# Kernel tuning notes

Measured on AMD Instinct MI355X. Metric: run time of the kernel, lower is better.

Reference implementation:

```python
import jax, jax.numpy as jnp
import numpy as np

B, C, D, T = 64, 512, 32, 32
DT = D * T
K = 128            # valid_num: top-K proposals kept for NMS-style pooling
MARGIN = 0.2       # opt.global_margin
MAX_VIOLATION = True
EPS = 1e-8         # torch.cosine_similarity eps


def _l2n(x, axis):
    # torch cosine_similarity normalizes each vector by max(||x||, eps)
    return x / jnp.maximum(jnp.linalg.norm(x, axis=axis, keepdims=True), EPS)


def _cos(a, b, axis):
    return jnp.sum(_l2n(a, axis) * _l2n(b, axis), axis=axis)


def setup_inputs() -> dict:
    key = jax.random.key(0)
    k1, k2, k3 = jax.random.split(key, 3)
    videos = jax.random.normal(k1, (B, C, D, T), jnp.float32)
    sentences = jax.random.normal(k2, (B, C), jnp.float32)
    iou = jax.random.uniform(k3, (DT, DT), jnp.float32)
    iou_maps = 0.5 * (iou + iou.T)
    iou_maps = iou_maps.at[jnp.arange(DT), jnp.arange(DT)].set(1.0)
    mask = jnp.ones((D, T), jnp.float32)
    lam = jnp.asarray(0.125, jnp.float32)
    return {"videos": videos, "sentences": sentences, "lam": lam,
            "mask": mask, "valid_num": K, "iou_maps": iou_maps}


def reference(videos, sentences, lam, mask, valid_num, iou_maps):
    b, c, d, t = videos.shape
    dt = d * t
    # center over channel dim (dim=1 in torch)
    V = videos - jnp.mean(videos, axis=1, keepdims=True)          # [b,c,d,t]
    S = sentences - jnp.mean(sentences, axis=1, keepdims=True)    # [b,c]
    Vf = V.reshape(b, c, dt)
    Vn = _l2n(Vf, axis=1)                                         # unit over c
    Sn = _l2n(S, axis=1)
    mflat = mask.reshape(dt)

    # cosine sim of every sentence vs every video proposal: [b_sent, b_vid, dt]
    cross = jnp.einsum('ic,jcp->ijp', Sn, Vn)
    cross = jnp.where(mflat == 0, -jnp.inf, cross)

    # --- per-sample positive pooling (loop 1) ---
    self_score = cross[jnp.arange(b), jnp.arange(b)]              # [b, dt]
    w = jax.nn.softmax(self_score, axis=-1)
    video_pos = jnp.einsum('bp,bcp->bc', w, Vf)                   # [b, c]

    # sentence-sentence sims + hard negative mining
    sim = Sn @ Sn.T                                               # [b, b]
    idx = jnp.argsort(-sim, axis=1)                               # descending
    neg_idx = idx[:, 6:b - 5]                                     # b > 11 path
    neg_sents = S[neg_idx]                                        # [b, b-11, c]
    pos_score = _cos(video_pos, S, axis=1)                        # [b]
    neg_score = _cos(video_pos[:, None, :], neg_sents, axis=2)    # [b, b-11]
    vas_loss = jnp.mean(jax.nn.relu(MARGIN + neg_score - pos_score[:, None]), axis=1).mean()

    # cross-video pseudo-positive (crov), gated on nearest-neighbor sim > 0.9
    nn_idx = idx[:, 1]
    pse = Vf[nn_idx]                                              # [b, c, dt]
    vsim = jax.nn.softmax(_cos(video_pos[:, :, None], pse, axis=1), axis=-1)  # [b, dt]
    p_v = jnp.einsum('bp,bcp->bc', vsim, pse)
    n_v = jnp.einsum('bp,bcp->bc', (1.0 - vsim) * mflat, pse) / (valid_num - 1)
    crov = jax.nn.relu(MARGIN + _cos(video_pos, n_v, axis=1) - _cos(video_pos, p_v, axis=1))
    gate = sim[jnp.arange(b), nn_idx] > 0.9
    crov_loss = jnp.where(gate, crov, 0.0).mean()

    # --- NMS-weighted video score pooling (loop 2) ---
    pmap = self_score.reshape(b, d, t)                            # postive_map
    topv, topi = jax.lax.top_k(cross, valid_num)                  # [b,b,K]
    # pairwise IoU among the top-K proposals of each (sentence, video) pair
    iou = iou_maps[topi[..., :, None], topi[..., None, :]]        # [b,b,K,K]
    lower = jnp.tril(jnp.ones((valid_num, valid_num), bool), -1)  # l < k
    decay = jnp.prod(1.0 - jnp.where(lower, iou, 0.0), axis=-1)   # [b,b,K]
    wk = jax.nn.softmax(lam * topv, axis=-1)
    scores = jnp.sum(wk * decay * topv, axis=-1)                  # [b,b]

    # bidirectional margin ranking loss
    diag = jnp.diag(scores)[:, None]
    eye = jnp.eye(b, dtype=bool)
    cost_s = jnp.where(eye, 0.0, jax.nn.relu(MARGIN + scores - diag))
    cost_im = jnp.where(eye, 0.0, jax.nn.relu(MARGIN + scores - diag.T))
    if MAX_VIOLATION:
        cost_s = cost_s.max(axis=1)
        cost_im = cost_im.max(axis=0)
    loss = cost_s.sum() / b + cost_im.sum() / b + vas_loss + crov_loss
    return loss, pmap
```

## Files before the change

kernel.cpp:

```cpp
#include <hip/hip_runtime.h>
#include <hip/hip_fp16.h>
#include <math.h>

#define BB 64
#define CC 512
#define DTT 1024
#define NNEG 53
#define MARGIN_ 0.2f
#define EPSV 1e-8f
#define LDB 132

typedef short s16x8 __attribute__((ext_vector_type(8)));
typedef float f32x4 __attribute__((ext_vector_type(4)));

__device__ __forceinline__ float bred_sum(float v, float* red, int tid, int nt) {
  red[tid] = v; __syncthreads();
  for (int s = nt >> 1; s > 0; s >>= 1) { if (tid < s) red[tid] += red[tid + s]; __syncthreads(); }
  float r = red[0]; __syncthreads();
  return r;
}
__device__ __forceinline__ float bred_max(float v, float* red, int tid, int nt) {
  red[tid] = v; __syncthreads();
  for (int s = nt >> 1; s > 0; s >>= 1) { if (tid < s) red[tid] = fmaxf(red[tid], red[tid + s]); __syncthreads(); }
  float r = red[0]; __syncthreads();
  return r;
}

__global__ void k_sent(const float* __restrict__ sent, float* __restrict__ Sn,
                       unsigned short* __restrict__ SnH, unsigned short* __restrict__ SnL,
                       float* __restrict__ SnSum) {
  int b = blockIdx.x, tid = threadIdx.x;
  __shared__ float red[256];
  float x0 = sent[b * CC + tid], x1 = sent[b * CC + tid + 256];
  float mean = bred_sum(x0 + x1, red, tid, 256) * (1.0f / CC);
  float s0 = x0 - mean, s1 = x1 - mean;
  float ss = bred_sum(s0 * s0 + s1 * s1, red, tid, 256);
  float nrm = fmaxf(sqrtf(ss), EPSV);
  float n0 = s0 / nrm, n1 = s1 / nrm;
  Sn[b * CC + tid] = n0; Sn[b * CC + tid + 256] = n1;
  unsigned u0 = __float_as_uint(n0), u1 = __float_as_uint(n1);
  SnH[b * CC + tid] = (unsigned short)(u0 >> 16);
  SnH[b * CC + tid + 256] = (unsigned short)(u1 >> 16);
  float l0 = n0 - __uint_as_float(u0 & 0xFFFF0000u);
  float l1 = n1 - __uint_as_float(u1 & 0xFFFF0000u);
  SnL[b * CC + tid] = (unsigned short)(__float_as_uint(l0) >> 16);
  SnL[b * CC + tid + 256] = (unsigned short)(__float_as_uint(l1) >> 16);
  float sn = bred_sum(n0 + n1, red, tid, 256);
  if (tid == 0) SnSum[b] = sn;
}

__global__ void k_sim(const float* __restrict__ Sn, int* __restrict__ nn_idx,
                      int* __restrict__ negidx, float* __restrict__ nnsim) {
  int i = blockIdx.x, j = threadIdx.x;
  float dot = 0.f;
  for (int c = 0; c < CC; ++c) dot += Sn[i * CC + c] * Sn[j * CC + c];
  __shared__ float srow[BB];
  srow[j] = dot; __syncthreads();
  float mv = srow[j];
  int rank = 0;
  for (int k = 0; k < BB; ++k) {
    float vk = srow[k];
    if (vk > mv || (vk == mv && k < j)) rank++;
  }
  if (rank == 1) { nn_idx[i] = j; nnsim[i] = mv; }
  if (rank >= 6 && rank < 59) negidx[i * NNEG + rank - 6] = j;
}

__global__ void k_prep_iou(const float* __restrict__ iou, __half* __restrict__ L16) {
  int g = (blockIdx.x * 256 + threadIdx.x) * 4;
  float4 x = *(const float4*)(iou + g);
  __half2 h0 = __floats2half2_rn(1.f - x.x, 1.f - x.y);
  __half2 h1 = __floats2half2_rn(1.f - x.z, 1.f - x.w);
  *(__half2*)(L16 + g) = h0;
  *(__half2*)(L16 + g + 2) = h1;
}

__global__ __launch_bounds__(256) void k_cross(const float* __restrict__ videos,
    const unsigned short* __restrict__ SnH, const unsigned short* __restrict__ SnL,
    const float* __restrict__ SnSum, const float* __restrict__ mask,
    float* __restrict__ cross, float* __restrict__ meanv, float* __restrict__ normv) {
  __shared__ unsigned int BH[2][16][LDB];
  __shared__ unsigned int BL[2][16][LDB];
  __shared__ float SnSum_s[64];
  __shared__ float mb_s[128];
  __shared__ float inv_s[128];

  int tid = threadIdx.x;
  int j = blockIdx.x >> 3;
  int p0 = (blockIdx.x & 7) << 7;
  int lane = tid & 63;
  int wv = tid >> 6;
  int row = lane & 15;
  int g = lane >> 4;
  int g8 = g << 3;
  int pA = wv << 5;

  int kp = tid >> 4;
  int pb = (tid & 15) << 3;

  const float* vbase = videos + ((size_t)j * CC) * DTT + p0;

  f32x4 acc[4][2];
#pragma unroll
  for (int a = 0; a < 4; ++a)
#pragma unroll
    for (int pf = 0; pf < 2; ++pf)
#pragma unroll
      for (int r = 0; r < 4; ++r) acc[a][pf][r] = 0.f;

  float sacc[8], ssacc[8];
#pragma unroll
  for (int q = 0; q < 8; ++q) { sacc[q] = 0.f; ssacc[q] = 0.f; }

  const float* pr = vbase + (size_t)(2 * kp) * DTT + pb;
  float4 f0 = *(const float4*)(pr);
  float4 f1 = *(const float4*)(pr + 4);
  float4 f2 = *(const float4*)(pr + DTT);
  float4 f3 = *(const float4*)(pr + DTT + 4);

#pragma unroll
  for (int t = 0; t < 16; ++t) {
    int kc = t * 32;
    int cb = t & 1;
    s16x8 AH[4], AL[4];
#pragma unroll
    for (int a = 0; a < 4; ++a) {
      int off = (a * 16 + row) * CC + kc + g8;
      AH[a] = *(const s16x8*)(SnH + off);
      AL[a] = *(const s16x8*)(SnL + off);
    }
    {
      float xe[8] = {f0.x, f0.y, f0.z, f0.w, f1.x, f1.y, f1.z, f1.w};
      float xo[8] = {f2.x, f2.y, f2.z, f2.w, f3.x, f3.y, f3.z, f3.w};
      unsigned int hw[8], lw[8];
#pragma unroll
      for (int q = 0; q < 8; ++q) {
        unsigned ue = __float_as_uint(xe[q]);
        unsigned uo = __float_as_uint(xo[q]);
        hw[q] = (ue >> 16) | (uo & 0xFFFF0000u);
        float el = xe[q] - __uint_as_float(ue & 0xFFFF0000u);
        float ol = xo[q] - __uint_as_float(uo & 0xFFFF0000u);
        lw[q] = (__float_as_uint(el) >> 16) | (__float_as_uint(ol) & 0xFFFF0000u);
        sacc[q] += xe[q] + xo[q];
        ssacc[q] = fmaf(xe[q], xe[q], ssacc[q]);
        ssacc[q] = fmaf(xo[q], xo[q], ssacc[q]);
      }
      *(uint4*)&BH[cb][kp][pb]     = make_uint4(hw[0], hw[1], hw[2], hw[3]);
      *(uint4*)&BH[cb][kp][pb + 4] = make_uint4(hw[4], hw[5], hw[6], hw[7]);
      *(uint4*)&BL[cb][kp][pb]     = make_uint4(lw[0], lw[1], lw[2], lw[3]);
      *(uint4*)&BL[cb][kp][pb + 4] = make_uint4(lw[4], lw[5], lw[6], lw[7]);
    }
    if (t + 1 < 16) {
      const float* pn = vbase + (size_t)((t + 1) * 32 + 2 * kp) * DTT + pb;
      f0 = *(const float4*)(pn);
      f1 = *(const float4*)(pn + 4);
      f2 = *(const float4*)(pn + DTT);
      f3 = *(const float4*)(pn + DTT + 4);
    }
    __syncthreads();
#pragma unroll
    for (int pf = 0; pf < 2; ++pf) {
      int p = pA + pf * 16 + row;
      int kpb = g << 2;
      union { unsigned int u[4]; s16x8 v; } bh, bl;
      bh.u[0] = BH[cb][kpb][p]; bh.u[1] = BH[cb][kpb + 1][p];
      bh.u[2] = BH[cb][kpb + 2][p]; bh.u[3] = BH[cb][kpb + 3][p];
      bl.u[0] = BL[cb][kpb][p]; bl.u[1] = BL[cb][kpb + 1][p];
      bl.u[2] = BL[cb][kpb + 2][p]; bl.u[3] = BL[cb][kpb + 3][p];
#pragma unroll
      for (int a = 0; a < 4; ++a) {
        acc[a][pf] = __builtin_amdgcn_mfma_f32_16x16x32_bf16(AH[a], bh.v, acc[a][pf], 0, 0, 0);
        acc[a][pf] = __builtin_amdgcn_mfma_f32_16x16x32_bf16(AH[a], bl.v, acc[a][pf], 0, 0, 0);
        acc[a][pf] = __builtin_amdgcn_mfma_f32_16x16x32_bf16(AL[a], bh.v, acc[a][pf], 0, 0, 0);
      }
    }
  }

  float (*Sred)[LDB] = (float(*)[LDB])&BH[0][0][0];
  float (*SSred)[LDB] = (float(*)[LDB])&BL[0][0][0];
#pragma unroll
  for (int q = 0; q < 8; ++q) { Sred[kp][pb + q] = sacc[q]; SSred[kp][pb + q] = ssacc[q]; }
  if (tid < 64) SnSum_s[tid] = SnSum[tid];
  __syncthreads();
  if (tid < 128) {
    float s = 0.f, ss = 0.f;
#pragma unroll
    for (int k = 0; k < 16; ++k) { s += Sred[k][tid]; ss += SSred[k][tid]; }
    float mb = s * (1.0f / CC);
    float var = ss - s * mb;
    float nrm = fmaxf(sqrtf(fmaxf(var, 0.f)), EPSV);
    meanv[j * DTT + p0 + tid] = mb;
    normv[j * DTT + p0 + tid] = nrm;
    mb_s[tid] = mb;
    inv_s[tid] = 1.f / nrm;
  }
  __syncthreads();

#pragma unroll
  for (int pf = 0; pf < 2; ++pf) {
    int p = pA + pf * 16 + row;
    float mb = mb_s[p], inv = inv_s[p];
    float mk = mask[p0 + p];
#pragma unroll
    for (int a = 0; a < 4; ++a) {
#pragma unroll
      for (int r = 0; r < 4; ++r) {
        int i = a * 16 + (g << 2) + r;
        float val = (acc[a][pf][r] - mb * SnSum_s[i]) * inv;
        if (mk == 0.f) val = -INFINITY;
        cross[((size_t)i * BB + j) * DTT + p0 + p] = val;
      }
    }
  }
}

__global__ void k_softmax_w(const float* __restrict__ cross, const float* __restrict__ meanv,
                            float* __restrict__ pmap, float* __restrict__ w, float* __restrict__ wm) {
  int b = blockIdx.x, tid = threadIdx.x;
  __shared__ float red[256];
  const float* row = cross + ((size_t)b * BB + b) * DTT;
  float v[4]; float mx = -INFINITY;
#pragma unroll
  for (int q = 0; q < 4; ++q) {
    v[q] = row[q * 256 + tid];
    pmap[b * DTT + q * 256 + tid] = v[q];
    mx = fmaxf(mx, v[q]);
  }
  mx = bred_max(mx, red, tid, 256);
  float e[4]; float se = 0.f;
#pragma unroll
  for (int q = 0; q < 4; ++q) { e[q] = expf(v[q] - mx); se += e[q]; }
  se = bred_sum(se, red, tid, 256);
  float inv = 1.f / se;
  float wmacc = 0.f;
#pragma unroll
  for (int q = 0; q < 4; ++q) {
    float wv = e[q] * inv;
    w[b * DTT + q * 256 + tid] = wv;
    wmacc += wv * meanv[b * DTT + q * 256 + tid];
  }
  wmacc = bred_sum(wmacc, red, tid, 256);
  if (tid == 0) wm[b] = wmacc;
}

__global__ void k_vpos(const float* __restrict__ videos, const float* __restrict__ w,
                       const float* __restrict__ wm, float* __restrict__ vp) {
  int wid = (blockIdx.x * 256 + threadIdx.x) >> 6;
  int lane = threadIdx.x & 63;
  int b = wid >> 9, c = wid & 511;
  const float4* vb = (const float4*)(videos + (size_t)(b * CC + c) * DTT) + lane * 4;
  const float4* wb = (const float4*)(w + b * DTT) + lane * 4;
  float acc = 0.f;
#pragma unroll
  for (int q = 0; q < 4; ++q) {
    float4 x = vb[q], y = wb[q];
    acc += x.x * y.x + x.y * y.y + x.z * y.z + x.w * y.w;
  }
#pragma unroll
  for (int off = 32; off > 0; off >>= 1) acc += __shfl_xor(acc, off);
  if (lane == 0) vp[b * CC + c] = acc - wm[b];
}

__global__ void k_vpnorm(const float* __restrict__ vp, float* __restrict__ vpn,
                         float* __restrict__ vpsum) {
  int b = blockIdx.x, tid = threadIdx.x;
  __shared__ float red[256];
  float x0 = vp[b * CC + tid], x1 = vp[b * CC + tid + 256];
  float ss = bred_sum(x0 * x0 + x1 * x1, red, tid, 256);
  float sm = bred_sum(x0 + x1, red, tid, 256);
  if (tid == 0) { vpn[b] = fmaxf(sqrtf(ss), EPSV); vpsum[b] = sm; }
}

__global__ void k_vsim_logits(const float* __restrict__ videos, const float* __restrict__ vp,
    const float* __restrict__ vpn, const float* __restrict__ vpsum, const int* __restrict__ nn_idx,
    const float* __restrict__ meanv, const float* __restrict__ normv, float* __restrict__ vslog) {
  int gid = blockIdx.x * 256 + threadIdx.x;
  int b = gid >> 10, p = gid & 1023;
  int nn = nn_idx[b];
  const float* base = videos + (size_t)nn * CC * DTT + p;
  const float* vpr = vp + b * CC;
  float acc = 0.f;
#pragma unroll 1
  for (int c0 = 0; c0 < CC; c0 += 16) {
    float v[16];
#pragma unroll
    for (int u = 0; u < 16; ++u) v[u] = base[(size_t)(c0 + u) * DTT];
#pragma unroll
    for (int u = 0; u < 16; ++u) acc = fmaf(vpr[c0 + u], v[u], acc);
  }
  acc -= meanv[nn * DTT + p] * vpsum[b];
  vslog[gid] = acc / (vpn[b] * normv[nn * DTT + p]);
}

__global__ void k_softmax_vsim(float* __restrict__ vslog, const int* __restrict__ nn_idx,
    const float* __restrict__ meanv, const float* __restrict__ mask,
    float* __restrict__ svp, float* __restrict__ svn) {
  int b = blockIdx.x, tid = threadIdx.x;
  __shared__ float red[256];
  int nn = nn_idx[b];
  float v[4]; float mx = -INFINITY;
#pragma unroll
  for (int q = 0; q < 4; ++q) { v[q] = vslog[b * DTT + q * 256 + tid]; mx = fmaxf(mx, v[q]); }
  mx = bred_max(mx, red, tid, 256);
  float e[4]; float se = 0.f;
#pragma unroll
  for (int q = 0; q < 4; ++q) { e[q] = expf(v[q] - mx); se += e[q]; }
  se = bred_sum(se, red, tid, 256);
  float inv = 1.f / se;
  float sp = 0.f, sn2 = 0.f;
#pragma unroll
  for (int q = 0; q < 4; ++q) {
    int p = q * 256 + tid;
    float vs = e[q] * inv;
    vslog[b * DTT + p] = vs;
    float mm = meanv[nn * DTT + p];
    sp += vs * mm;
    sn2 += (1.f - vs) * mask[p] * mm;
  }
  sp = bred_sum(sp, red, tid, 256);
  sn2 = bred_sum(sn2, red, tid, 256);
  if (tid == 0) { svp[b] = sp; svn[b] = sn2; }
}

__global__ void k_pvnv(const float* __restrict__ videos, const float* __restrict__ vsim,
    const int* __restrict__ nn_idx, const float* __restrict__ mask,
    const float* __restrict__ svp, const float* __restrict__ svn, const int* __restrict__ vn_p,
    float* __restrict__ pv, float* __restrict__ nv) {
  int wid = (blockIdx.x * 256 + threadIdx.x) >> 6;
  int lane = threadIdx.x & 63;
  int b = wid >> 9, c = wid & 511;
  int nn = nn_idx[b];
  const float4* vb = (const float4*)(videos + (size_t)(nn * CC + c) * DTT) + lane * 4;
  const float4* vs4 = (const float4*)(vsim + b * DTT) + lane * 4;
  const float4* m4 = ((const float4*)mask) + lane * 4;
  float ap = 0.f, an = 0.f;
#pragma unroll
  for (int q = 0; q < 4; ++q) {
    float4 x = vb[q], s = vs4[q], m = m4[q];
    ap += x.x * s.x + x.y * s.y + x.z * s.z + x.w * s.w;
    an += x.x * (1.f - s.x) * m.x + x.y * (1.f - s.y) * m.y + x.z * (1.f - s.z) * m.z + x.w * (1.f - s.w) * m.w;
  }
#pragma unroll
  for (int off = 32; off > 0; off >>= 1) { ap += __shfl_xor(ap, off); an += __shfl_xor(an, off); }
  if (lane == 0) {
    float kd = (float)(*vn_p - 1);
    pv[b * CC + c] = ap - svp[b];
    nv[b * CC + c] = (an - svn[b]) / kd;
  }
}

__global__ void k_vas(const float* __restrict__ vp, const float* __restrict__ vpn,
                      const float* __restrict__ Sn, const int* __restrict__ negidx,
                      float* __restrict__ vasrow) {
  int i = blockIdx.x, tid = threadIdx.x;
  __shared__ float red[64];
  __shared__ float pos;
  float invn = 1.f / vpn[i];
  float val = 0.f;
  if (tid < NNEG) {
    int nj = negidx[i * NNEG + tid];
    float d = 0.f;
    for (int c = 0; c < CC; ++c) d += vp[i * CC + c] * Sn[nj * CC + c];
    val = d * invn;
  }
  if (tid == 63) {
    float d = 0.f;
    for (int c = 0; c < CC; ++c) d += vp[i * CC + c] * Sn[i * CC + c];
    pos = d * invn;
  }
  __syncthreads();
  float contrib = (tid < NNEG) ? fmaxf(MARGIN_ + val - pos, 0.f) : 0.f;
  float s = bred_sum(contrib, red, tid, 64);
  if (tid == 0) vasrow[i] = s / (float)NNEG;
}

__global__ void k_crov(const float* __restrict__ vp, const float* __restrict__ vpn,
                       const float* __restrict__ pv, const float* __restrict__ nv,
                       const float* __restrict__ nnsim, float* __restrict__ crovrow) {
  int b = blockIdx.x, tid = threadIdx.x;
  __shared__ float red[256];
  float dp = 0.f, pp = 0.f, dn = 0.f, nn2 = 0.f;
  for (int c = tid; c < CC; c += 256) {
    float a = vp[b * CC + c], x = pv[b * CC + c], y = nv[b * CC + c];
    dp += a * x; pp += x * x; dn += a * y; nn2 += y * y;
  }
  dp = bred_sum(dp, red, tid, 256);
  pp = bred_sum(pp, red, tid, 256);
  dn = bred_sum(dn, red, tid, 256);
  nn2 = bred_sum(nn2, red, tid, 256);
  if (tid == 0) {
    float cosp = dp / (vpn[b] * fmaxf(sqrtf(pp), EPSV));
    float cosn = dn / (vpn[b] * fmaxf(sqrtf(nn2), EPSV));
    float crov = fmaxf(MARGIN_ + cosn - cosp, 0.f);
    crovrow[b] = (nnsim[b] > 0.9f) ? crov : 0.f;
  }
}

__global__ __launch_bounds__(256) void k_select(const float* __restrict__ cross,
    const int* __restrict__ vn_p, unsigned* __restrict__ ordi_g, float* __restrict__ ordv_g) {
  __shared__ unsigned int hist_s[4][256];
  __shared__ unsigned int sel_s[4][128];
  __shared__ unsigned int selk_s[4][128];
  __shared__ unsigned int cnt_s[4];
  int tid = threadIdx.x;
  int wv = tid >> 6, lane = tid & 63;
  int ij = blockIdx.x * 4 + wv;
  int K = *vn_p; if (K > 128) K = 128;
  unsigned int* hist = hist_s[wv];
  unsigned int* sel = sel_s[wv];
  unsigned int* selk = selk_s[wv];

  const float* row = cross + (size_t)ij * DTT;
  unsigned int v[16];
#pragma unroll
  for (int q = 0; q < 16; ++q) {
    unsigned u = __float_as_uint(row[q * 64 + lane]);
    v[q] = (u & 0x80000000u) ? ~u : (u | 0x80000000u);
  }
  if (lane == 0) cnt_s[wv] = 0u;
  __builtin_amdgcn_wave_barrier();

  unsigned prefix = 0u, pmask = 0u;
  int remaining = K;
  for (int shift = 24; shift >= 0; shift -= 8) {
#pragma unroll
    for (int q = 0; q < 4; ++q) hist[lane * 4 + q] = 0u;
    __builtin_amdgcn_wave_barrier();
#pragma unroll
    for (int q = 0; q < 16; ++q) {
      if ((v[q] & pmask) == prefix)
        atomicAdd(&hist[(v[q] >> shift) & 255u], 1u);
    }
    __builtin_amdgcn_wave_barrier();
    unsigned c0 = hist[lane * 4], c1 = hist[lane * 4 + 1];
    unsigned c2 = hist[lane * 4 + 2], c3 = hist[lane * 4 + 3];
    unsigned s = c0 + c1 + c2 + c3;
    unsigned inc = s;
#pragma unroll
    for (int off = 1; off < 64; off <<= 1) {
      unsigned t = __shfl_down(inc, off);
      if (lane + off < 64) inc += t;
    }
    unsigned exc = inc - s;
    bool found = (exc < (unsigned)remaining) && (inc >= (unsigned)remaining);
    unsigned long long bmask = __ballot(found);
    int winner = (int)(__ffsll((unsigned long long)bmask) - 1);
    unsigned packed = 0u;
    if (found) {
      unsigned c = exc;
      unsigned cc[4] = {c0, c1, c2, c3};
      int d = lane * 4;
#pragma unroll
      for (int q = 3; q >= 0; --q) {
        if (c + cc[q] >= (unsigned)remaining) { d = lane * 4 + q; break; }
        c += cc[q];
      }
      packed = ((unsigned)d << 16) | (unsigned)(remaining - (int)c);
    }
    packed = __shfl(packed, winner);
    prefix |= (packed >> 16) << shift;
    remaining = (int)(packed & 0xFFFFu);
    pmask |= 255u << shift;
  }

#pragma unroll
  for (int q = 0; q < 16; ++q) {
    if (v[q] > prefix) {
      unsigned pos = atomicAdd(&cnt_s[wv], 1u);
      sel[pos] = (unsigned)(q * 64 + lane);
      selk[pos] = v[q];
    }
  }
  __builtin_amdgcn_wave_barrier();
  {
    int base = K - remaining;
    int last = -1;
    for (int t = 0; t < remaining; ++t) {
      int mymin = 0x7FFFFFFF;
#pragma unroll
      for (int q = 0; q < 16; ++q) {
        int idx = q * 64 + lane;
        if (v[q] == prefix && idx > last && idx < mymin) mymin = idx;
      }
#pragma unroll
      for (int off = 32; off > 0; off >>= 1) mymin = min(mymin, __shfl_xor(mymin, off));
      if (lane == 0) { sel[base + t] = (unsigned)mymin; selk[base + t] = prefix; }
      last = mymin;
    }
  }
  __builtin_amdgcn_wave_barrier();

  for (int e = lane; e < K; e += 64) {
    unsigned myidx = sel[e], myk = selk[e];
    int rank = 0;
    for (int m = 0; m < K; ++m) {
      unsigned ok = selk[m];
      rank += (ok > myk || (ok == myk && sel[m] < myidx)) ? 1 : 0;
    }
    unsigned u = (myk & 0x80000000u) ? (myk & 0x7FFFFFFFu) : ~myk;
    ordi_g[ij * 128 + rank] = myidx;
    ordv_g[ij * 128 + rank] = __uint_as_float(u);
  }
}

__global__ __launch_bounds__(256) void k_decay(const __half* __restrict__ L16,
    const unsigned* __restrict__ ordi_g, const float* __restrict__ ordv_g,
    const float* __restrict__ lam_p, const int* __restrict__ vn_p,
    float* __restrict__ scores) {
  __shared__ unsigned ti[128];
  __shared__ float dks[128];
  int ij = blockIdx.x, tid = threadIdx.x;
  int wv = tid >> 6, lane = tid & 63;
  int K = *vn_p; if (K > 128) K = 128;
  float lam = *lam_p;
  if (tid < 128) {
    ti[tid] = (tid < K) ? ordi_g[ij * 128 + tid] : 0u;
    dks[tid] = 1.f;
  }
  __syncthreads();

  for (int r = wv; r < K; r += 4) {
    const __half* irow = L16 + (size_t)ti[r] * DTT;
    float f = 1.f;
    if (lane < r && lane < 64) f = __half2float(irow[ti[lane]]);
    float prod = f;
#pragma unroll
    for (int off = 32; off > 0; off >>= 1) prod *= __shfl_xor(prod, off);
    if (r > 64 && prod > 1e-14f) {
      float f2 = 1.f;
      int m = 64 + lane;
      if (m < r) f2 = __half2float(irow[ti[m]]);
#pragma unroll
      for (int off = 32; off > 0; off >>= 1) f2 *= __shfl_xor(f2, off);
      prod *= f2;
    }
    if (lane == 0) dks[r] = prod;
  }
  __syncthreads();

  if (wv == 0) {
    bool okA = (lane < K), okB = (lane + 64 < K);
    float vA = okA ? ordv_g[ij * 128 + lane] : 0.f;
    float vB = okB ? ordv_g[ij * 128 + lane + 64] : 0.f;
    float mx = fmaxf(okA ? lam * vA : -INFINITY, okB ? lam * vB : -INFINITY);
#pragma unroll
    for (int off = 32; off > 0; off >>= 1) mx = fmaxf(mx, __shfl_xor(mx, off));
    float eA = okA ? expf(lam * vA - mx) : 0.f;
    float eB = okB ? expf(lam * vB - mx) : 0.f;
    float se = eA + eB;
    float sc = (okA ? eA * dks[lane] * vA : 0.f) + (okB ? eB * dks[lane + 64] * vB : 0.f);
#pragma unroll
    for (int off = 32; off > 0; off >>= 1) {
      se += __shfl_xor(se, off);
      sc += __shfl_xor(sc, off);
    }
    if (lane == 0) scores[ij] = sc / se;
  }
}

__global__ void k_final(const float* __restrict__ scores, const float* __restrict__ vasrow,
                        const float* __restrict__ crovrow, float* __restrict__ out) {
  int tid = threadIdx.x;
  __shared__ float sm[BB * BB];
  __shared__ float red[64];
  for (int q = tid; q < BB * BB; q += 64) sm[q] = scores[q];
  __syncthreads();
  float di = sm[tid * BB + tid];
  float rowmax = 0.f, colmax = 0.f;
  for (int k = 0; k < BB; ++k) {
    if (k != tid) {
      rowmax = fmaxf(rowmax, fmaxf(MARGIN_ + sm[tid * BB + k] - di, 0.f));
      colmax = fmaxf(colmax, fmaxf(MARGIN_ + sm[k * BB + tid] - di, 0.f));
    }
  }
  float total = bred_sum(rowmax + colmax + vasrow[tid] + crovrow[tid], red, tid, 64);
  if (tid == 0) out[0] = total * (1.0f / BB);
}

extern "C" void kernel_launch(void* const* d_in, const int* in_sizes, int n_in,
                              void* d_out, int out_size, void* d_ws, size_t ws_size,
                              hipStream_t stream) {
  const float* videos = (const float*)d_in[0];
  const float* sentences = (const float*)d_in[1];
  const float* lam = (const float*)d_in[2];
  const float* mask = (const float*)d_in[3];
  const int* valid_num = (const int*)d_in[4];
  const float* iou_maps = (const float*)d_in[5];
  float* out = (float*)d_out;
  float* pmap = out + 1;

  float* ws = (float*)d_ws;
  float* Sn = ws;
  float* SnT_unused = Sn + 32768;
  float* SnSum = SnT_unused + 32768;
  float* meanv = SnSum + 64;
  float* normv = meanv + 65536;
  float* cross = normv + 65536;
  float* w = cross + 4194304;
  float* wm = w + 65536;
  float* vp = wm + 64;
  float* vpn = vp + 32768;
  float* vpsum = vpn + 64;
  float* nnsim = vpsum + 64;
  float* vslog = nnsim + 64;
  float* svp = vslog + 65536;
  float* svn = svp + 64;
  float* pvb = svn + 64;
  float* nvb = pvb + 32768;
  float* vasrow = nvb + 32768;
  float* crovrow = vasrow + 64;
  float* scores = crovrow + 64;
  int* nn_idx = (int*)(scores + 4096);
  int* negidx = nn_idx + 64;
  unsigned* ordi_g = (unsigned*)(negidx + 3392);
  float* ordv_g = (float*)(ordi_g + 524288);
  __half* L16 = (__half*)(ordv_g + 524288);
  unsigned short* SnH16 = (unsigned short*)(L16 + 1048576);
  unsigned short* SnL16 = SnH16 + 32768;

  k_sent<<<64, 256, 0, stream>>>(sentences, Sn, SnH16, SnL16, SnSum);
  k_sim<<<64, 64, 0, stream>>>(Sn, nn_idx, negidx, nnsim);
  k_prep_iou<<<1024, 256, 0, stream>>>(iou_maps, L16);
  k_cross<<<512, 256, 0, stream>>>(videos, SnH16, SnL16, SnSum, mask, cross, meanv, normv);
  k_softmax_w<<<64, 256, 0, stream>>>(cross, meanv, pmap, w, wm);
  k_vpos<<<8192, 256, 0, stream>>>(videos, w, wm, vp);
  k_vpnorm<<<64, 256, 0, stream>>>(vp, vpn, vpsum);
  k_vsim_logits<<<256, 256, 0, stream>>>(videos, vp, vpn, vpsum, nn_idx, meanv, normv, vslog);
  k_softmax_vsim<<<64, 256, 0, stream>>>(vslog, nn_idx, meanv, mask, svp, svn);
  k_pvnv<<<8192, 256, 0, stream>>>(videos, vslog, nn_idx, mask, svp, svn, valid_num, pvb, nvb);
  k_vas<<<64, 64, 0, stream>>>(vp, vpn, Sn, negidx, vasrow);
  k_crov<<<64, 256, 0, stream>>>(vp, vpn, pvb, nvb, nnsim, crovrow);
  k_select<<<1024, 256, 0, stream>>>(cross, valid_num, ordi_g, ordv_g);
  k_decay<<<4096, 256, 0, stream>>>(L16, ordi_g, ordv_g, lam, valid_num, scores);
  k_final<<<1, 64, 0, stream>>>(scores, vasrow, crovrow, out);
}
```

Baseline: 435.3 us.

## Halve cross-sim position tile and restructure NMS decay via shared IoU tile

The cross-similarity kernel now processes 64 proposals per block instead of 128, doubling the grid to raise occupancy and parallelism at the cost of reloading the sentence operand more often. The decay kernel first gathers the lower-triangular pairwise (1-IoU) entries into a shared half-precision tile, then computes each row's product with one thread per row instead of wave-wide shuffle reductions. This drops the early-exit for near-zero products and adds a large shared-memory footprint and uneven per-thread loop lengths.

```diff
diff --git a/kernel.cpp b/kernel.cpp
--- a/kernel.cpp
+++ b/kernel.cpp
@@ -8,7 +8,7 @@
 #define NNEG 53
 #define MARGIN_ 0.2f
 #define EPSV 1e-8f
-#define LDB 132
+#define LDB2 68
 
 typedef short s16x8 __attribute__((ext_vector_type(8)));
 typedef float f32x4 __attribute__((ext_vector_type(4)));
@@ -79,44 +79,40 @@
     const unsigned short* __restrict__ SnH, const unsigned short* __restrict__ SnL,
     const float* __restrict__ SnSum, const float* __restrict__ mask,
     float* __restrict__ cross, float* __restrict__ meanv, float* __restrict__ normv) {
-  __shared__ unsigned int BH[2][16][LDB];
-  __shared__ unsigned int BL[2][16][LDB];
+  __shared__ unsigned int BH[2][16][LDB2];
+  __shared__ unsigned int BL[2][16][LDB2];
   __shared__ float SnSum_s[64];
-  __shared__ float mb_s[128];
-  __shared__ float inv_s[128];
+  __shared__ float mb_s[64];
+  __shared__ float inv_s[64];
 
   int tid = threadIdx.x;
-  int j = blockIdx.x >> 3;
-  int p0 = (blockIdx.x & 7) << 7;
+  int j = blockIdx.x >> 4;
+  int p0 = (blockIdx.x & 15) << 6;
   int lane = tid & 63;
   int wv = tid >> 6;
   int row = lane & 15;
   int g = lane >> 4;
   int g8 = g << 3;
-  int pA = wv << 5;
+  int pA = wv << 4;
 
   int kp = tid >> 4;
-  int pb = (tid & 15) << 3;
+  int pb = (tid & 15) << 2;
 
   const float* vbase = videos + ((size_t)j * CC) * DTT + p0;
 
-  f32x4 acc[4][2];
+  f32x4 acc[4];
 #pragma unroll
   for (int a = 0; a < 4; ++a)
 #pragma unroll
-    for (int pf = 0; pf < 2; ++pf)
-#pragma unroll
-      for (int r = 0; r < 4; ++r) acc[a][pf][r] = 0.f;
-
-  float sacc[8], ssacc[8];
-#pragma unroll
-  for (int q = 0; q < 8; ++q) { sacc[q] = 0.f; ssacc[q] = 0.f; }
+    for (int r = 0; r < 4; ++r) acc[a][r] = 0.f;
+
+  float sacc[4], ssacc[4];
+#pragma unroll
+  for (int q = 0; q < 4; ++q) { sacc[q] = 0.f; ssacc[q] = 0.f; }
 
   const float* pr = vbase + (size_t)(2 * kp) * DTT + pb;
   float4 f0 = *(const float4*)(pr);
-  float4 f1 = *(const float4*)(pr + 4);
   float4 f2 = *(const float4*)(pr + DTT);
-  float4 f3 = *(const float4*)(pr + DTT + 4);
 
 #pragma unroll
   for (int t = 0; t < 16; ++t) {
@@ -130,11 +126,11 @@
       AL[a] = *(const s16x8*)(SnL + off);
     }
     {
-      float xe[8] = {f0.x, f0.y, f0.z, f0.w, f1.x, f1.y, f1.z, f1.w};
-      float xo[8] = {f2.x, f2.y, f2.z, f2.w, f3.x, f3.y, f3.z, f3.w};
-      unsigned int hw[8], lw[8];
-#pragma unroll
-      for (int q = 0; q < 8; ++q) {
+      float xe[4] = {f0.x, f0.y, f0.z, f0.w};
+      float xo[4] = {f2.x, f2.y, f2.z, f2.w};
+      unsigned int hw[4], lw[4];
+#pragma unroll
+      for (int q = 0; q < 4; ++q) {
         unsigned ue = __float_as_uint(xe[q]);
         unsigned uo = __float_as_uint(xo[q]);
         hw[q] = (ue >> 16) | (uo & 0xFFFF0000u);
@@ -145,22 +141,17 @@
         ssacc[q] = fmaf(xe[q], xe[q], ssacc[q]);
         ssacc[q] = fmaf(xo[q], xo[q], ssacc[q]);
       }
-      *(uint4*)&BH[cb][kp][pb]     = make_uint4(hw[0], hw[1], hw[2], hw[3]);
-      *(uint4*)&BH[cb][kp][pb + 4] = make_uint4(hw[4], hw[5], hw[6], hw[7]);
-      *(uint4*)&BL[cb][kp][pb]     = make_uint4(lw[0], lw[1], lw[2], lw[3]);
-      *(uint4*)&BL[cb][kp][pb + 4] = make_uint4(lw[4], lw[5], lw[6], lw[7]);
+      *(uint4*)&BH[cb][kp][pb] = make_uint4(hw[0], hw[1], hw[2], hw[3]);
+      *(uint4*)&BL[cb][kp][pb] = make_uint4(lw[0], lw[1], lw[2], lw[3]);
     }
     if (t + 1 < 16) {
       const float* pn = vbase + (size_t)((t + 1) * 32 + 2 * kp) * DTT + pb;
       f0 = *(const float4*)(pn);
-      f1 = *(const float4*)(pn + 4);
       f2 = *(const float4*)(pn + DTT);
-      f3 = *(const float4*)(pn + DTT + 4);
     }
     __syncthreads();
-#pragma unroll
-    for (int pf = 0; pf < 2; ++pf) {
-      int p = pA + pf * 16 + row;
+    {
+      int p = pA + row;
       int kpb = g << 2;
       union { unsigned int u[4]; s16x8 v; } bh, bl;
       bh.u[0] = BH[cb][kpb][p]; bh.u[1] = BH[cb][kpb + 1][p];
@@ -169,20 +160,20 @@
       bl.u[2] = BL[cb][kpb + 2][p]; bl.u[3] = BL[cb][kpb + 3][p];
 #pragma unroll
       for (int a = 0; a < 4; ++a) {
-        acc[a][pf] = __builtin_amdgcn_mfma_f32_16x16x32_bf16(AH[a], bh.v, acc[a][pf], 0, 0, 0);
-        acc[a][pf] = __builtin_amdgcn_mfma_f32_16x16x32_bf16(AH[a], bl.v, acc[a][pf], 0, 0, 0);
-        acc[a][pf] = __builtin_amdgcn_mfma_f32_16x16x32_bf16(AL[a], bh.v, acc[a][pf], 0, 0, 0);
+        acc[a] = __builtin_amdgcn_mfma_f32_16x16x32_bf16(AH[a], bh.v, acc[a], 0, 0, 0);
+        acc[a] = __builtin_amdgcn_mfma_f32_16x16x32_bf16(AH[a], bl.v, acc[a], 0, 0, 0);
+        acc[a] = __builtin_amdgcn_mfma_f32_16x16x32_bf16(AL[a], bh.v, acc[a], 0, 0, 0);
       }
     }
   }
 
-  float (*Sred)[LDB] = (float(*)[LDB])&BH[0][0][0];
-  float (*SSred)[LDB] = (float(*)[LDB])&BL[0][0][0];
-#pragma unroll
-  for (int q = 0; q < 8; ++q) { Sred[kp][pb + q] = sacc[q]; SSred[kp][pb + q] = ssacc[q]; }
+  float (*Sred)[LDB2] = (float(*)[LDB2])&BH[0][0][0];
+  float (*SSred)[LDB2] = (float(*)[LDB2])&BL[0][0][0];
+#pragma unroll
+  for (int q = 0; q < 4; ++q) { Sred[kp][pb + q] = sacc[q]; SSred[kp][pb + q] = ssacc[q]; }
   if (tid < 64) SnSum_s[tid] = SnSum[tid];
   __syncthreads();
-  if (tid < 128) {
+  if (tid < 64) {
     float s = 0.f, ss = 0.f;
 #pragma unroll
     for (int k = 0; k < 16; ++k) { s += Sred[k][tid]; ss += SSred[k][tid]; }
@@ -196,9 +187,8 @@
   }
   __syncthreads();
 
-#pragma unroll
-  for (int pf = 0; pf < 2; ++pf) {
-    int p = pA + pf * 16 + row;
+  {
+    int p = pA + row;
     float mb = mb_s[p], inv = inv_s[p];
     float mk = mask[p0 + p];
 #pragma unroll
@@ -206,7 +196,7 @@
 #pragma unroll
       for (int r = 0; r < 4; ++r) {
         int i = a * 16 + (g << 2) + r;
-        float val = (acc[a][pf][r] - mb * SnSum_s[i]) * inv;
+        float val = (acc[a][r] - mb * SnSum_s[i]) * inv;
         if (mk == 0.f) val = -INFINITY;
         cross[((size_t)i * BB + j) * DTT + p0 + p] = val;
       }
@@ -508,33 +498,42 @@
     const float* __restrict__ lam_p, const int* __restrict__ vn_p,
     float* __restrict__ scores) {
   __shared__ unsigned ti[128];
+  __shared__ __half Lt[128][132];
   __shared__ float dks[128];
   int ij = blockIdx.x, tid = threadIdx.x;
   int wv = tid >> 6, lane = tid & 63;
   int K = *vn_p; if (K > 128) K = 128;
   float lam = *lam_p;
-  if (tid < 128) {
-    ti[tid] = (tid < K) ? ordi_g[ij * 128 + tid] : 0u;
-    dks[tid] = 1.f;
-  }
+  if (tid < 128) ti[tid] = (tid < 128) ? ((tid < K) ? ordi_g[ij * 128 + tid] : 0u) : 0u;
   __syncthreads();
 
   for (int r = wv; r < K; r += 4) {
     const __half* irow = L16 + (size_t)ti[r] * DTT;
-    float f = 1.f;
-    if (lane < r && lane < 64) f = __half2float(irow[ti[lane]]);
-    float prod = f;
-#pragma unroll
-    for (int off = 32; off > 0; off >>= 1) prod *= __shfl_xor(prod, off);
-    if (r > 64 && prod > 1e-14f) {
-      float f2 = 1.f;
-      int m = 64 + lane;
-      if (m < r) f2 = __half2float(irow[ti[m]]);
-#pragma unroll
-      for (int off = 32; off > 0; off >>= 1) f2 *= __shfl_xor(f2, off);
-      prod *= f2;
-    }
-    if (lane == 0) dks[r] = prod;
+    if (lane < r) Lt[r][lane] = irow[ti[lane]];
+    int m = 64 + lane;
+    if (m < r) Lt[r][m] = irow[ti[m]];
+  }
+  __syncthreads();
+
+  if (tid < 128) {
+    float prod = 1.f;
+    if (tid < K && tid > 0) {
+      int r = tid;
+      const __half* rowp = &Lt[r][0];
+      float pa = 1.f, pb2 = 1.f;
+      int m = 0;
+      for (; m + 8 <= r; m += 8) {
+        float2 a = __half22float2(*(const __half2*)&rowp[m]);
+        float2 b = __half22float2(*(const __half2*)&rowp[m + 2]);
+        float2 c = __half22float2(*(const __half2*)&rowp[m + 4]);
+        float2 d = __half22float2(*(const __half2*)&rowp[m + 6]);
+        pa *= a.x * a.y; pb2 *= b.x * b.y;
+        pa *= c.x * c.y; pb2 *= d.x * d.y;
+      }
+      for (; m < r; ++m) pa *= __half2float(rowp[m]);
+      prod = pa * pb2;
+    }
+    dks[tid] = prod;
   }
   __syncthreads();
 
@@ -621,7 +620,7 @@
   k_sent<<<64, 256, 0, stream>>>(sentences, Sn, SnH16, SnL16, SnSum);
   k_sim<<<64, 64, 0, stream>>>(Sn, nn_idx, negidx, nnsim);
   k_prep_iou<<<1024, 256, 0, stream>>>(iou_maps, L16);
-  k_cross<<<512, 256, 0, stream>>>(videos, SnH16, SnL16, SnSum, mask, cross, meanv, normv);
+  k_cross<<<1024, 256, 0, stream>>>(videos, SnH16, SnL16, SnSum, mask, cross, meanv, normv);
   k_softmax_w<<<64, 256, 0, stream>>>(cross, meanv, pmap, w, wm);
   k_vpos<<<8192, 256, 0, stream>>>(videos, w, wm, vp);
   k_vpnorm<<<64, 256, 0, stream>>>(vp, vpn, vpsum);
```

After: 475.5 us. 9.2% more time.
